# Optimization experiments

Measured on AMD Instinct MI355X. Metric: run time of the kernel, lower is better.

The kernel has to match this reference:

```python
import jax, jax.numpy as jnp
import numpy as np

C = 512        # feat_dim
T_LEN = 8192   # sequence length
N = 16384      # number of proposals
HID = 1024     # hidden_dim
OUT = 512      # out_dim
RATIO = 0.15   # boundary_ratio


def setup_inputs() -> dict:
    key = jax.random.key(0)
    ks = jax.random.split(key, 6)
    feat_map = jax.random.normal(ks[0], (C, T_LEN), jnp.float32)
    l = jax.random.randint(ks[1], (N,), 0, T_LEN - 64)
    width = jax.random.randint(ks[2], (N,), 8, 512)
    r = jnp.minimum(l + width, T_LEN - 1)
    W1 = jax.random.normal(ks[3], (HID, 2 * C), jnp.float32) * 0.02
    b1 = jnp.zeros((HID,), jnp.float32)
    W2 = jax.random.normal(ks[4], (OUT, HID), jnp.float32) * 0.02
    b2 = jnp.zeros((OUT,), jnp.float32)
    return {
        "feat_map": feat_map,
        "l": l.astype(jnp.int32),
        "r": r.astype(jnp.int32),
        "T": T_LEN,
        "W1": W1, "b1": b1, "W2": W2, "b2": b2,
    }


def _boundary_regions(l, r, T):
    # Mirrors: w = max(r-l, 1.0); bw = max(1, int(ratio*w)); clipped windows.
    lf = l.astype(jnp.float32)
    rf = r.astype(jnp.float32)
    w = jnp.maximum(rf - lf, 1.0)
    bw = jnp.maximum(1, (RATIO * w).astype(jnp.int32))  # int() truncation (w > 0)
    rl = jnp.round(lf).astype(jnp.int32)
    rr = jnp.round(rf).astype(jnp.int32)
    lb_s = jnp.maximum(0, rl - bw)
    lb_e = jnp.minimum(T, rl + bw)
    rb_s = jnp.maximum(0, rr - bw)
    rb_e = jnp.minimum(T, rr + bw)
    return lb_s, lb_e, rb_s, rb_e


def _pool(cs, s, e, T):
    # mean of feat[:, s:e] via inclusive prefix sums; cs: (C, T+1)
    e = jnp.maximum(s + 1, e)
    e = jnp.minimum(e, T)
    seg = cs[:, e] - cs[:, s]                      # (C, N)
    return (seg / (e - s).astype(cs.dtype)).T      # (N, C)


def reference(feat_map, l, r, T, W1, b1, W2, b2):
    # feat_map: (C, T); l, r: (N,) int proposal boundaries
    cs = jnp.concatenate(
        [jnp.zeros((feat_map.shape[0], 1), feat_map.dtype),
         jnp.cumsum(feat_map, axis=1)], axis=1)    # (C, T+1)
    lb_s, lb_e, rb_s, rb_e = _boundary_regions(l, r, T)
    e_left = _pool(cs, lb_s, lb_e, T)              # (N, C)
    e_right = _pool(cs, rb_s, rb_e, T)             # (N, C)
    e = jnp.concatenate([e_left, e_right], axis=-1)  # (N, 2C)
    h = jax.nn.relu(e @ W1.T + b1)                 # (N, HID)
    return h @ W2.T + b2                           # (N, OUT)
```

## Files before the change

### kernel.cpp

```cpp
#include <hip/hip_runtime.h>
#include <hip/hip_bf16.h>
#include <stdint.h>

#define C_DIM 512
#define T_SEQ 8192
#define N_PROP 16384
#define HID_DIM 1024
#define OUT_DIM 512
#define K2C 1024

typedef __attribute__((ext_vector_type(8))) __bf16 bf16x8;
typedef __attribute__((ext_vector_type(4))) float f32x4;

__global__ __launch_bounds__(64) void cumsum_kernel(const float* __restrict__ feat,
                                                    float* __restrict__ cs_inc) {
    int c = blockIdx.x;
    const float4* in = (const float4*)(feat + (size_t)c * T_SEQ);
    float4* out = (float4*)(cs_inc + (size_t)c * T_SEQ);
    int lane = threadIdx.x;
    float carry = 0.0f;
    for (int i0 = 0; i0 < T_SEQ / 4; i0 += 64) {
        float4 v = in[i0 + lane];
        float s1 = v.x + v.y;
        float s2 = s1 + v.z;
        float s3 = s2 + v.w;
        float x = s3;
#pragma unroll
        for (int s = 1; s < 64; s <<= 1) {
            float y = __shfl_up(x, s);
            if (lane >= s) x += y;
        }
        float base = carry + (x - s3);
        float4 o;
        o.x = base + v.x; o.y = base + s1; o.z = base + s2; o.w = base + s3;
        out[i0 + lane] = o;
        carry += __shfl(x, 63);
    }
}

__global__ __launch_bounds__(256) void transpose_kernel(const float* __restrict__ cs_inc,
                                                        float* __restrict__ cs_t) {
    __shared__ float tl[32][33];
    int tx = threadIdx.x, ty = threadIdx.y;
    int x0 = blockIdx.x * 32;
    int y0 = blockIdx.y * 32;
#pragma unroll
    for (int i = 0; i < 32; i += 8) {
        int t = x0 + tx;
        int ch = y0 + ty + i;
        float v = 0.0f;
        if (t >= 1 && t <= T_SEQ) v = cs_inc[(size_t)ch * T_SEQ + (t - 1)];
        tl[ty + i][tx] = v;
    }
    __syncthreads();
#pragma unroll
    for (int i = 0; i < 32; i += 8) {
        int t = x0 + ty + i;
        int ch = y0 + tx;
        if (t <= T_SEQ) cs_t[(size_t)t * C_DIM + ch] = tl[tx][ty + i];
    }
}

__global__ __launch_bounds__(512) void pool_kernel(const float* __restrict__ cs_t,
                                                   const int* __restrict__ lptr,
                                                   const int* __restrict__ rptr,
                                                   __hip_bfloat16* __restrict__ e) {
    int n = blockIdx.x * 4 + (threadIdx.x >> 7);
    int c4 = (threadIdx.x & 127) * 4;
    int li = lptr[n], ri = rptr[n];
    float w = fmaxf((float)(ri - li), 1.0f);
    int bw = max(1, (int)(0.15f * w));
    int lb_s = max(0, li - bw);
    int lb_e = min(T_SEQ, li + bw);
    int rb_s = max(0, ri - bw);
    int rb_e = min(T_SEQ, ri + bw);
    lb_e = min(max(lb_s + 1, lb_e), T_SEQ);
    rb_e = min(max(rb_s + 1, rb_e), T_SEQ);
    float4 a = *(const float4*)(cs_t + (size_t)lb_e * C_DIM + c4);
    float4 b = *(const float4*)(cs_t + (size_t)lb_s * C_DIM + c4);
    float4 cc = *(const float4*)(cs_t + (size_t)rb_e * C_DIM + c4);
    float4 d = *(const float4*)(cs_t + (size_t)rb_s * C_DIM + c4);
    float rl = 1.0f / (float)(lb_e - lb_s);
    float rr = 1.0f / (float)(rb_e - rb_s);
    __hip_bfloat16 L0 = __float2bfloat16((a.x - b.x) * rl);
    __hip_bfloat16 L1 = __float2bfloat16((a.y - b.y) * rl);
    __hip_bfloat16 L2 = __float2bfloat16((a.z - b.z) * rl);
    __hip_bfloat16 L3 = __float2bfloat16((a.w - b.w) * rl);
    __hip_bfloat16 R0 = __float2bfloat16((cc.x - d.x) * rr);
    __hip_bfloat16 R1 = __float2bfloat16((cc.y - d.y) * rr);
    __hip_bfloat16 R2 = __float2bfloat16((cc.z - d.z) * rr);
    __hip_bfloat16 R3 = __float2bfloat16((cc.w - d.w) * rr);
    ushort4 ul, ur;
    ul.x = *(unsigned short*)&L0; ul.y = *(unsigned short*)&L1;
    ul.z = *(unsigned short*)&L2; ul.w = *(unsigned short*)&L3;
    ur.x = *(unsigned short*)&R0; ur.y = *(unsigned short*)&R1;
    ur.z = *(unsigned short*)&R2; ur.w = *(unsigned short*)&R3;
    *(ushort4*)(e + (size_t)n * K2C + c4) = ul;
    *(ushort4*)(e + (size_t)n * K2C + C_DIM + c4) = ur;
}

__global__ __launch_bounds__(256) void cvt_bf16_kernel(const float* __restrict__ W1,
                                                       const float* __restrict__ W2,
                                                       __hip_bfloat16* __restrict__ W1b,
                                                       __hip_bfloat16* __restrict__ W2b) {
    const int n1 = HID_DIM * K2C;
    int i = (blockIdx.x * 256 + threadIdx.x) * 4;
    const float* src;
    __hip_bfloat16* dst;
    int j;
    if (i < n1) { src = W1; dst = W1b; j = i; }
    else        { src = W2; dst = W2b; j = i - n1; }
    float4 v = *(const float4*)(src + j);
    __hip_bfloat16 h0 = __float2bfloat16(v.x);
    __hip_bfloat16 h1 = __float2bfloat16(v.y);
    __hip_bfloat16 h2 = __float2bfloat16(v.z);
    __hip_bfloat16 h3 = __float2bfloat16(v.w);
    ushort4 u;
    u.x = *(unsigned short*)&h0; u.y = *(unsigned short*)&h1;
    u.z = *(unsigned short*)&h2; u.w = *(unsigned short*)&h3;
    *(ushort4*)(dst + j) = u;
}

template <int BM, int BN, int WM, int WN, int NSLOT, int K, int RELU_BF16>
__global__ __launch_bounds__(512, 2) void gemm_dp_kernel(const __hip_bfloat16* __restrict__ A,
                                                         const __hip_bfloat16* __restrict__ B,
                                                         const float* __restrict__ bias,
                                                         void* __restrict__ Cout,
                                                         int Nc, int NBlk) {
    constexpr int BK = 64;
    constexpr int NT = K / BK;
    constexpr int WMT = BM / WM, WNT = BN / WN;
    constexpr int MR = WMT / 16, NR = WNT / 16;
    constexpr int LA = BM / 64, LB = BN / 64;
    constexpr int LPT = LA + LB;

    __shared__ __align__(16) __hip_bfloat16 As[NSLOT][BM * BK];
    __shared__ __align__(16) __hip_bfloat16 Bs[NSLOT][BN * BK];

    const int tid = threadIdx.x;
    const int lane = tid & 63;
    const int wid = tid >> 6;
    const int wm = wid / WN;
    const int wn = wid % WN;

    const int nwg = gridDim.x;
    const int wg = (blockIdx.x & 7) * (nwg >> 3) + (blockIdx.x >> 3);
    const long m0 = (long)(wg / NBlk) * BM;
    const long n0 = (long)(wg % NBlk) * BN;

    const int srow = tid >> 3;
    const int schunk = (tid & 7) ^ (srow & 7);
    const int fr = lane & 15;
    const int g8 = (lane >> 4) * 8;

    f32x4 acc[MR][NR] = {};

    auto stage = [&](int s, int k0) {
#pragma unroll
        for (int i = 0; i < LA; ++i)
            __builtin_amdgcn_global_load_lds(
                (const __attribute__((address_space(1))) void*)(A + (m0 + i * 64 + srow) * K + k0 + schunk * 8),
                (__attribute__((address_space(3))) void*)(&As[s][i * 4096 + tid * 8]), 16, 0, 0);
#pragma unroll
        for (int i = 0; i < LB; ++i)
            __builtin_amdgcn_global_load_lds(
                (const __attribute__((address_space(1))) void*)(B + (n0 + i * 64 + srow) * K + k0 + schunk * 8),
                (__attribute__((address_space(3))) void*)(&Bs[s][i * 4096 + tid * 8]), 16, 0, 0);
    };
    auto ldA = [&](int s, int row, int kbase) -> bf16x8 {
        return *(const bf16x8*)(&As[s][row * BK + ((kbase + g8) ^ ((row & 7) * 8))]);
    };
    auto ldB = [&](int s, int row, int kbase) -> bf16x8 {
        return *(const bf16x8*)(&Bs[s][row * BK + ((kbase + g8) ^ ((row & 7) * 8))]);
    };

#pragma unroll
    for (int s = 0; s < NSLOT; ++s) stage(s, s * BK);
    asm volatile("s_waitcnt vmcnt(%0)" ::"n"(LPT * (NSLOT - 1)) : "memory");
    __builtin_amdgcn_s_barrier();

    for (int u = 0; u < NT; ++u) {
        const int cur = u % NSLOT;
        bf16x8 af[MR], bv[NR];
#pragma unroll
        for (int m = 0; m < MR; ++m) af[m] = ldA(cur, wm * WMT + m * 16 + fr, 0);
#pragma unroll
        for (int n = 0; n < NR; ++n) bv[n] = ldB(cur, wn * WNT + n * 16 + fr, 0);
        __builtin_amdgcn_s_setprio(1);
#pragma unroll
        for (int m = 0; m < MR; ++m)
#pragma unroll
            for (int n = 0; n < NR; ++n)
                acc[m][n] = __builtin_amdgcn_mfma_f32_16x16x32_bf16(af[m], bv[n], acc[m][n], 0, 0, 0);
        __builtin_amdgcn_s_setprio(0);
#pragma unroll
        for (int m = 0; m < MR; ++m) af[m] = ldA(cur, wm * WMT + m * 16 + fr, 32);
#pragma unroll
        for (int n = 0; n < NR; ++n) bv[n] = ldB(cur, wn * WNT + n * 16 + fr, 32);
        __builtin_amdgcn_s_setprio(1);
#pragma unroll
        for (int m = 0; m < MR; ++m)
#pragma unroll
            for (int n = 0; n < NR; ++n)
                acc[m][n] = __builtin_amdgcn_mfma_f32_16x16x32_bf16(af[m], bv[n], acc[m][n], 0, 0, 0);
        __builtin_amdgcn_s_setprio(0);

        __builtin_amdgcn_s_barrier();
        if (u + NSLOT < NT) stage(cur, (u + NSLOT) * BK);
        if (u + 1 < NT) {
            if (u + NSLOT < NT)
                asm volatile("s_waitcnt vmcnt(%0)" ::"n"(LPT * (NSLOT - 1)) : "memory");
            else if (NSLOT == 3 && u + 2 < NT)
                asm volatile("s_waitcnt vmcnt(%0)" ::"n"(LPT) : "memory");
            else
                asm volatile("s_waitcnt vmcnt(0)" ::: "memory");
            __builtin_amdgcn_s_barrier();
        }
    }

    const int rq = (lane >> 4) * 4;
#pragma unroll
    for (int m = 0; m < MR; ++m)
#pragma unroll
        for (int n = 0; n < NR; ++n) {
            long col = n0 + wn * WNT + n * 16 + fr;
            float bb = bias[col];
#pragma unroll
            for (int q = 0; q < 4; ++q) {
                long row = m0 + wm * WMT + m * 16 + rq + q;
                float v = acc[m][n][q] + bb;
                if (RELU_BF16) {
                    v = fmaxf(v, 0.0f);
                    ((__hip_bfloat16*)Cout)[row * Nc + col] = __float2bfloat16(v);
                } else {
                    ((float*)Cout)[row * Nc + col] = v;
                }
            }
        }
}

extern "C" void kernel_launch(void* const* d_in, const int* in_sizes, int n_in,
                              void* d_out, int out_size, void* d_ws, size_t ws_size,
                              hipStream_t stream) {
    const float* feat = (const float*)d_in[0];
    const int* l = (const int*)d_in[1];
    const int* r = (const int*)d_in[2];
    const float* W1 = (const float*)d_in[4];
    const float* b1 = (const float*)d_in[5];
    const float* W2 = (const float*)d_in[6];
    const float* b2 = (const float*)d_in[7];

    char* ws = (char*)d_ws;
    float* cs_t = (float*)ws;
    __hip_bfloat16* e = (__hip_bfloat16*)(ws + 16779264);
    __hip_bfloat16* h = (__hip_bfloat16*)(ws + 50333696);
    float* cs_inc = (float*)(ws + 50333696);
    __hip_bfloat16* W1b = (__hip_bfloat16*)(ws + 83888128);
    __hip_bfloat16* W2b = (__hip_bfloat16*)(ws + 85985280);

    const int ncvt = (HID_DIM * K2C + OUT_DIM * HID_DIM) / 4 / 256;
    cvt_bf16_kernel<<<dim3(ncvt), 256, 0, stream>>>(W1, W2, W1b, W2b);
    cumsum_kernel<<<dim3(C_DIM), 64, 0, stream>>>(feat, cs_inc);
    transpose_kernel<<<dim3((T_SEQ + 32) / 32, C_DIM / 32), dim3(32, 8), 0, stream>>>(cs_inc, cs_t);
    pool_kernel<<<dim3(N_PROP / 4), 512, 0, stream>>>(cs_t, l, r, e);

    gemm_dp_kernel<256, 256, 2, 4, 2, K2C, 1>
        <<<dim3((N_PROP / 256) * (HID_DIM / 256)), 512, 0, stream>>>(e, W1b, b1, h, HID_DIM, HID_DIM / 256);
    gemm_dp_kernel<256, 128, 4, 2, 3, HID_DIM, 0>
        <<<dim3((N_PROP / 256) * (OUT_DIM / 128)), 512, 0, stream>>>(h, W2b, b2, d_out, OUT_DIM, OUT_DIM / 128);
}
```

Baseline: 112.9 us.

## Rewrite GEMM main loop as 8-phase interleaved load/MFMA schedule

Replaces the simple double/triple-buffered GEMM loop with a two-slot, eight-phase schedule. Each phase splits the MFMA work into half-M chunks and interleaves LDS reads and global-to-LDS prefetch chunks between barriers, with sched_barrier fences to pin the ordering. The goal is to hide global-load and LDS latency behind matrix-core work and to keep the MFMA units busy continuously. In exchange it adds many more barriers per k-step, and the hand-counted vmcnt waits are fragile if the tile configuration changes.

```diff
diff --git a/kernel.cpp b/kernel.cpp
--- a/kernel.cpp
+++ b/kernel.cpp
@@ -11,6 +11,10 @@
 
 typedef __attribute__((ext_vector_type(8))) __bf16 bf16x8;
 typedef __attribute__((ext_vector_type(4))) float f32x4;
+
+#define BARRIER() __builtin_amdgcn_s_barrier()
+#define SBAR() __builtin_amdgcn_sched_barrier(0)
+#define LGKM0() asm volatile("s_waitcnt lgkmcnt(0)" ::: "memory")
 
 __global__ __launch_bounds__(64) void cumsum_kernel(const float* __restrict__ feat,
                                                     float* __restrict__ cs_inc) {
@@ -121,21 +125,25 @@
     *(ushort4*)(dst + j) = u;
 }
 
-template <int BM, int BN, int WM, int WN, int NSLOT, int K, int RELU_BF16>
-__global__ __launch_bounds__(512, 2) void gemm_dp_kernel(const __hip_bfloat16* __restrict__ A,
-                                                         const __hip_bfloat16* __restrict__ B,
-                                                         const float* __restrict__ bias,
-                                                         void* __restrict__ Cout,
-                                                         int Nc, int NBlk) {
+template <int BM, int BN, int WM, int WN, int K, int RELU_BF16>
+__global__ __launch_bounds__(512, 2) void gemm8f_kernel(const __hip_bfloat16* __restrict__ A,
+                                                        const __hip_bfloat16* __restrict__ B,
+                                                        const float* __restrict__ bias,
+                                                        void* __restrict__ Cout,
+                                                        int Nc, int NBlk) {
     constexpr int BK = 64;
     constexpr int NT = K / BK;
+    constexpr int NI = NT / 2;
     constexpr int WMT = BM / WM, WNT = BN / WN;
     constexpr int MR = WMT / 16, NR = WNT / 16;
+    constexpr int MH = MR / 2;
     constexpr int LA = BM / 64, LB = BN / 64;
     constexpr int LPT = LA + LB;
-
-    __shared__ __align__(16) __hip_bfloat16 As[NSLOT][BM * BK];
-    __shared__ __align__(16) __hip_bfloat16 Bs[NSLOT][BN * BK];
+    constexpr int TC = LPT - 4;
+    constexpr int TCa = TC - TC / 2, TCb = TC / 2;
+
+    __shared__ __align__(16) __hip_bfloat16 As[2][BM * BK];
+    __shared__ __align__(16) __hip_bfloat16 Bs[2][BN * BK];
 
     const int tid = threadIdx.x;
     const int lane = tid & 63;
@@ -155,17 +163,15 @@
 
     f32x4 acc[MR][NR] = {};
 
-    auto stage = [&](int s, int k0) {
-#pragma unroll
-        for (int i = 0; i < LA; ++i)
+    auto stage_one = [&](int s, long k0, int j) {
+        if (j < LA)
             __builtin_amdgcn_global_load_lds(
-                (const __attribute__((address_space(1))) void*)(A + (m0 + i * 64 + srow) * K + k0 + schunk * 8),
-                (__attribute__((address_space(3))) void*)(&As[s][i * 4096 + tid * 8]), 16, 0, 0);
-#pragma unroll
-        for (int i = 0; i < LB; ++i)
+                (const __attribute__((address_space(1))) void*)(A + (m0 + j * 64 + srow) * K + k0 + schunk * 8),
+                (__attribute__((address_space(3))) void*)(&As[s][j * 4096 + tid * 8]), 16, 0, 0);
+        else
             __builtin_amdgcn_global_load_lds(
-                (const __attribute__((address_space(1))) void*)(B + (n0 + i * 64 + srow) * K + k0 + schunk * 8),
-                (__attribute__((address_space(3))) void*)(&Bs[s][i * 4096 + tid * 8]), 16, 0, 0);
+                (const __attribute__((address_space(1))) void*)(B + (n0 + (j - LA) * 64 + srow) * K + k0 + schunk * 8),
+                (__attribute__((address_space(3))) void*)(&Bs[s][(j - LA) * 4096 + tid * 8]), 16, 0, 0);
     };
     auto ldA = [&](int s, int row, int kbase) -> bf16x8 {
         return *(const bf16x8*)(&As[s][row * BK + ((kbase + g8) ^ ((row & 7) * 8))]);
@@ -174,48 +180,89 @@
         return *(const bf16x8*)(&Bs[s][row * BK + ((kbase + g8) ^ ((row & 7) * 8))]);
     };
 
-#pragma unroll
-    for (int s = 0; s < NSLOT; ++s) stage(s, s * BK);
-    asm volatile("s_waitcnt vmcnt(%0)" ::"n"(LPT * (NSLOT - 1)) : "memory");
-    __builtin_amdgcn_s_barrier();
-
-    for (int u = 0; u < NT; ++u) {
-        const int cur = u % NSLOT;
-        bf16x8 af[MR], bv[NR];
-#pragma unroll
-        for (int m = 0; m < MR; ++m) af[m] = ldA(cur, wm * WMT + m * 16 + fr, 0);
-#pragma unroll
-        for (int n = 0; n < NR; ++n) bv[n] = ldB(cur, wn * WNT + n * 16 + fr, 0);
+    bf16x8 af0[MR], af1[MR], bv0[NR], bv1[NR];
+
+    auto rd = [&](int s, int kb, bf16x8* af, bf16x8* bv) {
+#pragma unroll
+        for (int m = 0; m < MR; ++m) af[m] = ldA(s, wm * WMT + m * 16 + fr, kb);
+#pragma unroll
+        for (int n = 0; n < NR; ++n) bv[n] = ldB(s, wn * WNT + n * 16 + fr, kb);
+    };
+    auto mf = [&](const bf16x8* af, const bf16x8* bv, int mlo) {
         __builtin_amdgcn_s_setprio(1);
 #pragma unroll
-        for (int m = 0; m < MR; ++m)
+        for (int m = 0; m < MH; ++m)
 #pragma unroll
             for (int n = 0; n < NR; ++n)
-                acc[m][n] = __builtin_amdgcn_mfma_f32_16x16x32_bf16(af[m], bv[n], acc[m][n], 0, 0, 0);
+                acc[mlo + m][n] =
+                    __builtin_amdgcn_mfma_f32_16x16x32_bf16(af[mlo + m], bv[n], acc[mlo + m][n], 0, 0, 0);
         __builtin_amdgcn_s_setprio(0);
-#pragma unroll
-        for (int m = 0; m < MR; ++m) af[m] = ldA(cur, wm * WMT + m * 16 + fr, 32);
-#pragma unroll
-        for (int n = 0; n < NR; ++n) bv[n] = ldB(cur, wn * WNT + n * 16 + fr, 32);
-        __builtin_amdgcn_s_setprio(1);
-#pragma unroll
-        for (int m = 0; m < MR; ++m)
-#pragma unroll
-            for (int n = 0; n < NR; ++n)
-                acc[m][n] = __builtin_amdgcn_mfma_f32_16x16x32_bf16(af[m], bv[n], acc[m][n], 0, 0, 0);
-        __builtin_amdgcn_s_setprio(0);
-
-        __builtin_amdgcn_s_barrier();
-        if (u + NSLOT < NT) stage(cur, (u + NSLOT) * BK);
-        if (u + 1 < NT) {
-            if (u + NSLOT < NT)
-                asm volatile("s_waitcnt vmcnt(%0)" ::"n"(LPT * (NSLOT - 1)) : "memory");
-            else if (NSLOT == 3 && u + 2 < NT)
-                asm volatile("s_waitcnt vmcnt(%0)" ::"n"(LPT) : "memory");
-            else
-                asm volatile("s_waitcnt vmcnt(0)" ::: "memory");
-            __builtin_amdgcn_s_barrier();
+    };
+
+#pragma unroll
+    for (int j = 0; j < LPT; ++j) stage_one(0, 0, j);
+#pragma unroll
+    for (int j = 0; j < 4; ++j) stage_one(1, BK, j);
+    asm volatile("s_waitcnt vmcnt(4)" ::: "memory");
+    BARRIER();
+
+#pragma unroll 1
+    for (int i = 0; i < NI; ++i) {
+        const long u1 = 2 * i + 1;
+        const bool sE = (2 * i + 2 < NT);
+        const bool sO = (2 * i + 3 < NT);
+        const long kE = (2 * i + 2) * BK, kO = (2 * i + 3) * BK, kU1 = u1 * BK;
+
+        rd(0, 0, af0, bv0);
+#pragma unroll
+        for (int j = 4; j < 4 + TCa; ++j) stage_one(1, kU1, j);
+        BARRIER(); SBAR();
+        mf(af0, bv0, 0);
+        BARRIER();
+        rd(0, 32, af1, bv1);
+#pragma unroll
+        for (int j = 4 + TCa; j < LPT; ++j) stage_one(1, kU1, j);
+        BARRIER(); SBAR();
+        mf(af0, bv0, MH);
+        LGKM0();
+        BARRIER();
+        if (sE) { stage_one(0, kE, 0); stage_one(0, kE, 1); }
+        BARRIER(); SBAR();
+        mf(af1, bv1, 0);
+        BARRIER();
+        if (sE) { stage_one(0, kE, 2); stage_one(0, kE, 3); }
+        BARRIER(); SBAR();
+        mf(af1, bv1, MH);
+        if (sE) asm volatile("s_waitcnt vmcnt(4)" ::: "memory");
+        else    asm volatile("s_waitcnt vmcnt(0)" ::: "memory");
+        BARRIER();
+        rd(1, 0, af0, bv0);
+        if (sE) {
+#pragma unroll
+            for (int j = 4; j < 4 + TCa; ++j) stage_one(0, kE, j);
         }
+        BARRIER(); SBAR();
+        mf(af0, bv0, 0);
+        BARRIER();
+        rd(1, 32, af1, bv1);
+        if (sE) {
+#pragma unroll
+            for (int j = 4 + TCa; j < LPT; ++j) stage_one(0, kE, j);
+        }
+        BARRIER(); SBAR();
+        mf(af0, bv0, MH);
+        LGKM0();
+        BARRIER();
+        if (sO) { stage_one(1, kO, 0); stage_one(1, kO, 1); }
+        BARRIER(); SBAR();
+        mf(af1, bv1, 0);
+        BARRIER();
+        if (sO) { stage_one(1, kO, 2); stage_one(1, kO, 3); }
+        BARRIER(); SBAR();
+        mf(af1, bv1, MH);
+        if (sO) asm volatile("s_waitcnt vmcnt(4)" ::: "memory");
+        else if (sE) asm volatile("s_waitcnt vmcnt(0)" ::: "memory");
+        BARRIER();
     }
 
     const int rq = (lane >> 4) * 4;
@@ -264,8 +311,8 @@
     transpose_kernel<<<dim3((T_SEQ + 32) / 32, C_DIM / 32), dim3(32, 8), 0, stream>>>(cs_inc, cs_t);
     pool_kernel<<<dim3(N_PROP / 4), 512, 0, stream>>>(cs_t, l, r, e);
 
-    gemm_dp_kernel<256, 256, 2, 4, 2, K2C, 1>
+    gemm8f_kernel<256, 256, 2, 4, K2C, 1>
         <<<dim3((N_PROP / 256) * (HID_DIM / 256)), 512, 0, stream>>>(e, W1b, b1, h, HID_DIM, HID_DIM / 256);
-    gemm_dp_kernel<256, 128, 4, 2, 3, HID_DIM, 0>
+    gemm8f_kernel<256, 128, 4, 2, HID_DIM, 0>
         <<<dim3((N_PROP / 256) * (OUT_DIM / 128)), 512, 0, stream>>>(h, W2b, b2, d_out, OUT_DIM, OUT_DIM / 128);
 }
```

Result: slower. 117.0 us (+3.6%).

## Merge weight conversion and cumsum into one kernel with 4-wave per-row scan

Applied to the files above, without the earlier changes.

Replaces the single-wave-per-channel cumsum with a 256-thread block in which four waves each scan a quarter of the row, then combine their partial sums through shared memory. The same launch also carries the weight bf16 conversion blocks, which removes one kernel launch. The cumsum gains more parallelism per row, since the old version ran one serial 64-lane loop. The cost is register pressure from holding eight float4 values per thread.

```diff
diff --git a/kernel.cpp b/kernel.cpp
--- a/kernel.cpp
+++ b/kernel.cpp
@@ -12,29 +12,65 @@
 typedef __attribute__((ext_vector_type(8))) __bf16 bf16x8;
 typedef __attribute__((ext_vector_type(4))) float f32x4;
 
-__global__ __launch_bounds__(64) void cumsum_kernel(const float* __restrict__ feat,
-                                                    float* __restrict__ cs_inc) {
-    int c = blockIdx.x;
-    const float4* in = (const float4*)(feat + (size_t)c * T_SEQ);
-    float4* out = (float4*)(cs_inc + (size_t)c * T_SEQ);
-    int lane = threadIdx.x;
-    float carry = 0.0f;
-    for (int i0 = 0; i0 < T_SEQ / 4; i0 += 64) {
-        float4 v = in[i0 + lane];
-        float s1 = v.x + v.y;
-        float s2 = s1 + v.z;
-        float s3 = s2 + v.w;
-        float x = s3;
-#pragma unroll
-        for (int s = 1; s < 64; s <<= 1) {
-            float y = __shfl_up(x, s);
-            if (lane >= s) x += y;
-        }
-        float base = carry + (x - s3);
-        float4 o;
-        o.x = base + v.x; o.y = base + s1; o.z = base + s2; o.w = base + s3;
-        out[i0 + lane] = o;
-        carry += __shfl(x, 63);
+__global__ __launch_bounds__(256) void pre_kernel(const float* __restrict__ feat,
+                                                  float* __restrict__ cs_inc,
+                                                  const float* __restrict__ W1,
+                                                  const float* __restrict__ W2,
+                                                  __hip_bfloat16* __restrict__ W1b,
+                                                  __hip_bfloat16* __restrict__ W2b) {
+    if (blockIdx.x < C_DIM) {
+        int c = blockIdx.x;
+        const float4* in = (const float4*)(feat + (size_t)c * T_SEQ);
+        float4* out = (float4*)(cs_inc + (size_t)c * T_SEQ);
+        const int lane = threadIdx.x & 63;
+        const int w = threadIdx.x >> 6;
+        __shared__ float wsum[4];
+        float4 v[8];
+        float carry = 0.0f;
+#pragma unroll
+        for (int i = 0; i < 8; ++i) {
+            float4 t = in[w * 512 + i * 64 + lane];
+            float a1 = t.x + t.y;
+            float a2 = a1 + t.z;
+            float a3 = a2 + t.w;
+            float x = a3;
+#pragma unroll
+            for (int s = 1; s < 64; s <<= 1) {
+                float y = __shfl_up(x, s);
+                if (lane >= s) x += y;
+            }
+            float base = carry + (x - a3);
+            v[i].x = base + t.x; v[i].y = base + a1; v[i].z = base + a2; v[i].w = base + a3;
+            carry += __shfl(x, 63);
+        }
+        if (lane == 0) wsum[w] = carry;
+        __syncthreads();
+        float pre = 0.0f;
+        for (int j = 0; j < 4; ++j)
+            if (j < w) pre += wsum[j];
+#pragma unroll
+        for (int i = 0; i < 8; ++i) {
+            float4 o;
+            o.x = v[i].x + pre; o.y = v[i].y + pre; o.z = v[i].z + pre; o.w = v[i].w + pre;
+            out[w * 512 + i * 64 + lane] = o;
+        }
+    } else {
+        const int n1 = HID_DIM * K2C;
+        int i = ((blockIdx.x - C_DIM) * 256 + threadIdx.x) * 4;
+        const float* src;
+        __hip_bfloat16* dst;
+        int j;
+        if (i < n1) { src = W1; dst = W1b; j = i; }
+        else        { src = W2; dst = W2b; j = i - n1; }
+        float4 v = *(const float4*)(src + j);
+        __hip_bfloat16 h0 = __float2bfloat16(v.x);
+        __hip_bfloat16 h1 = __float2bfloat16(v.y);
+        __hip_bfloat16 h2 = __float2bfloat16(v.z);
+        __hip_bfloat16 h3 = __float2bfloat16(v.w);
+        ushort4 u;
+        u.x = *(unsigned short*)&h0; u.y = *(unsigned short*)&h1;
+        u.z = *(unsigned short*)&h2; u.w = *(unsigned short*)&h3;
+        *(ushort4*)(dst + j) = u;
     }
 }
 
@@ -99,28 +135,6 @@
     *(ushort4*)(e + (size_t)n * K2C + C_DIM + c4) = ur;
 }
 
-__global__ __launch_bounds__(256) void cvt_bf16_kernel(const float* __restrict__ W1,
-                                                       const float* __restrict__ W2,
-                                                       __hip_bfloat16* __restrict__ W1b,
-                                                       __hip_bfloat16* __restrict__ W2b) {
-    const int n1 = HID_DIM * K2C;
-    int i = (blockIdx.x * 256 + threadIdx.x) * 4;
-    const float* src;
-    __hip_bfloat16* dst;
-    int j;
-    if (i < n1) { src = W1; dst = W1b; j = i; }
-    else        { src = W2; dst = W2b; j = i - n1; }
-    float4 v = *(const float4*)(src + j);
-    __hip_bfloat16 h0 = __float2bfloat16(v.x);
-    __hip_bfloat16 h1 = __float2bfloat16(v.y);
-    __hip_bfloat16 h2 = __float2bfloat16(v.z);
-    __hip_bfloat16 h3 = __float2bfloat16(v.w);
-    ushort4 u;
-    u.x = *(unsigned short*)&h0; u.y = *(unsigned short*)&h1;
-    u.z = *(unsigned short*)&h2; u.w = *(unsigned short*)&h3;
-    *(ushort4*)(dst + j) = u;
-}
-
 template <int BM, int BN, int WM, int WN, int NSLOT, int K, int RELU_BF16>
 __global__ __launch_bounds__(512, 2) void gemm_dp_kernel(const __hip_bfloat16* __restrict__ A,
                                                          const __hip_bfloat16* __restrict__ B,
@@ -259,8 +273,7 @@
     __hip_bfloat16* W2b = (__hip_bfloat16*)(ws + 85985280);
 
     const int ncvt = (HID_DIM * K2C + OUT_DIM * HID_DIM) / 4 / 256;
-    cvt_bf16_kernel<<<dim3(ncvt), 256, 0, stream>>>(W1, W2, W1b, W2b);
-    cumsum_kernel<<<dim3(C_DIM), 64, 0, stream>>>(feat, cs_inc);
+    pre_kernel<<<dim3(C_DIM + ncvt), 256, 0, stream>>>(feat, cs_inc, W1, W2, W1b, W2b);
     transpose_kernel<<<dim3((T_SEQ + 32) / 32, C_DIM / 32), dim3(32, 8), 0, stream>>>(cs_inc, cs_t);
     pool_kernel<<<dim3(N_PROP / 4), 512, 0, stream>>>(cs_t, l, r, e);
 
```

Measured after the change: 105.2 us (median of 2 runs). 6.8% less time.
